# Kernel optimization log

Hardware: AMD Instinct MI355X
Metric: run time of the kernel (lower is better)

## Reference

```python
import jax, jax.numpy as jnp
import numpy as np

K = 10          # neighbors, hard-coded in MLP1.forward
NEG_SLOPE = 0.2 # LeakyReLU slope
EPS = 1e-5      # BatchNorm2d default eps


def setup_inputs() -> dict:
    key = jax.random.key(0)
    k1, k2, k3, k4 = jax.random.split(key, 4)
    B, C, N = 8, 6, 4096
    x = jax.random.normal(k1, (B, C, N), dtype=jnp.float32)
    W = jax.random.normal(k2, (64, 6), dtype=jnp.float32) * 0.2      # conv1x1 weight (O, I)
    gamma = jax.random.uniform(k3, (64,), jnp.float32, 0.5, 1.5)     # BN weight
    beta = jax.random.normal(k4, (64,), dtype=jnp.float32) * 0.1     # BN bias
    return {"x": x, "W": W, "gamma": gamma, "beta": beta}


def _knn_idx(x3, k):
    # pairwise_distance[b,i,j] = -||x_i - x_j||^2 (as in the torch knn)
    inner = jnp.einsum('bdn,bdm->bnm', x3, x3)          # x_i . x_j
    xx = jnp.sum(x3 * x3, axis=1)                       # (B, N)
    pd = 2.0 * inner - xx[:, :, None] - xx[:, None, :]  # (B, N, N)
    _, idx = jax.lax.top_k(pd, k)                       # k nearest (incl. self)
    return idx                                          # (B, N, k) int32


def reference(x, W, gamma, beta):
    # x: (B, 6, N)
    idx = _knn_idx(x[:, :3], K)                          # (B, N, k)
    # gather neighbor features: feat[b,c,n,j] = x[b,c,idx[b,n,j]]
    feat = jax.vmap(lambda xb, ib: xb[:, ib])(x, idx)    # (B, 6, N, k)
    # center xyz over the k neighbors and scale by 10
    xyz = feat[:, :3]
    xyz = (xyz - jnp.mean(xyz, axis=-1, keepdims=True)) * 10.0
    feat = jnp.concatenate([xyz, feat[:, 3:]], axis=1)   # (B, 6, N, k)
    # 1x1 conv (6 -> 64), no bias
    y = jnp.einsum('oc,bcnk->bonk', W, feat)             # (B, 64, N, k)
    # BatchNorm2d in train mode: batch stats over (B, N, k), biased variance
    mu = jnp.mean(y, axis=(0, 2, 3), keepdims=True)
    var = jnp.mean((y - mu) ** 2, axis=(0, 2, 3), keepdims=True)
    y = (y - mu) * jax.lax.rsqrt(var + EPS)
    y = y * gamma[None, :, None, None] + beta[None, :, None, None]
    # LeakyReLU(0.2)
    y = jnp.where(y >= 0, y, NEG_SLOPE * y)
    # max over neighbors k
    y = jnp.max(y, axis=-1)                              # (B, 64, N)
    # global max + mean pooling over N, concat along last axis
    x1 = jnp.max(y, axis=-1)                             # (B, 64)
    x2 = jnp.mean(y, axis=-1)                            # (B, 64)
    return jnp.concatenate([x1, x2], axis=-1)            # (B, 128)
```

## Files before the change

kernel.cpp:

```cpp
#include <hip/hip_runtime.h>
#include <float.h>

#define K_NN 10
#define BATCH 8
#define CIN 6
#define NPTS 4096
#define COUT 64
#define NSEG 8
#define SEGLEN (NPTS / NSEG)
#define CHUNK 16
#define NCHUNK (SEGLEN / CHUNK)
#define CAP 32
#define TPP 8
#define PPB2 32
#define SCAP 80
#define NEG_SLOPE 0.2f
#define BN_EPS 1e-5f

static constexpr size_t OFF_PTS2 = 0;
static constexpr size_t OFF_PTS  = OFF_PTS2 + (size_t)BATCH * NPTS * sizeof(float4);
static constexpr size_t OFF_Q    = OFF_PTS + (size_t)BATCH * NPTS * sizeof(float4);
static constexpr size_t SZ_Q     = (size_t)BATCH * NSEG * K_NN * NPTS * sizeof(int);
static constexpr size_t OFF_ST   = OFF_Q + SZ_Q;

__device__ __forceinline__ float wave_sum(float v) {
#pragma unroll
    for (int m = 32; m >= 1; m >>= 1) v += __shfl_xor(v, m, 64);
    return v;
}
__device__ __forceinline__ float wave_max(float v) {
#pragma unroll
    for (int m = 32; m >= 1; m >>= 1) v = fmaxf(v, __shfl_xor(v, m, 64));
    return v;
}

__device__ __forceinline__ float distp3(float qdx, float qdy, float qdz, float4 c) {
    return fmaf(qdx, c.x, fmaf(qdy, c.y, fmaf(qdz, c.z, -c.w)));
}

__device__ __forceinline__ void lex_insert(float (&vals)[K_NN], int (&inds)[K_NN],
                                           float d, int m) {
    if (d > vals[K_NN - 1] || (d == vals[K_NN - 1] && m < inds[K_NN - 1])) {
        vals[K_NN - 1] = d;
        inds[K_NN - 1] = m;
#pragma unroll
        for (int t = K_NN - 1; t > 0; t--) {
            if (vals[t] > vals[t - 1] ||
                (vals[t] == vals[t - 1] && inds[t] < inds[t - 1])) {
                float tv = vals[t]; vals[t] = vals[t - 1]; vals[t - 1] = tv;
                int ti = inds[t]; inds[t] = inds[t - 1]; inds[t - 1] = ti;
            }
        }
    }
}

__global__ __launch_bounds__(256) void prep_pts(const float* __restrict__ x,
                                                float4* __restrict__ pts,
                                                float4* __restrict__ pts2,
                                                double* __restrict__ stats) {
    if (blockIdx.x == 0 && threadIdx.x < 27) stats[threadIdx.x] = 0.0;
    int t = blockIdx.x * 256 + threadIdx.x;
    int b = t >> 12;
    int n = t & (NPTS - 1);
    const float* xb = x + (size_t)b * CIN * NPTS;
    float x0 = xb[n];
    float x1 = xb[NPTS + n];
    float x2 = xb[2 * NPTS + n];
    pts[t] = make_float4(x0, x1, x2, x0 * x0 + x1 * x1 + x2 * x2);
    pts2[t] = make_float4(xb[3 * NPTS + n], xb[4 * NPTS + n], xb[5 * NPTS + n], 0.f);
}

__global__ __launch_bounds__(256) void knn_part(const float4* __restrict__ pts,
                                                int* __restrict__ part) {
    __shared__ unsigned short ssm[CAP * 256];
    int b = blockIdx.y;
    int s = blockIdx.z;
    int n = blockIdx.x * 256 + threadIdx.x;
    const float4* p = pts + (size_t)b * NPTS;
    float4 qp = p[n];
    float qdx = 2.0f * qp.x, qdy = 2.0f * qp.y, qdz = 2.0f * qp.z;

    int m0 = s * SEGLEN;

    float vals[K_NN];
#pragma unroll
    for (int j = 0; j < K_NN; j++) vals[j] = -FLT_MAX;

    for (int ch = 0; ch < NCHUNK; ch++) {
        float cmax = -FLT_MAX;
#pragma unroll
        for (int u = 0; u < CHUNK; u++) {
            float4 c = p[m0 + ch * CHUNK + u];
            cmax = fmaxf(cmax, distp3(qdx, qdy, qdz, c));
        }
        float t = cmax;
#pragma unroll
        for (int j = 0; j < K_NN; j++) {
            float hi = fmaxf(vals[j], t);
            t = fminf(vals[j], t);
            vals[j] = hi;
        }
    }
    float thr = vals[K_NN - 1];

    int cnt = 0;
#pragma unroll 8
    for (int mm = 0; mm < SEGLEN; mm++) {
        float4 c = p[m0 + mm];
        float d = distp3(qdx, qdy, qdz, c);
        int slot = min(cnt, CAP - 1);
        ssm[slot * 256 + threadIdx.x] = (unsigned short)(m0 + mm);
        cnt += (d >= thr) ? 1 : 0;
    }

    float fv[K_NN];
    int fi[K_NN];
#pragma unroll
    for (int j = 0; j < K_NN; j++) { fv[j] = -FLT_MAX; fi[j] = 0; }

    if (cnt <= CAP) {
        for (int j = 0; j < cnt; j++) {
            int m = ssm[j * 256 + threadIdx.x];
            float4 c = p[m];
            float d = distp3(qdx, qdy, qdz, c);
            if (d > fv[K_NN - 1]) {
                fv[K_NN - 1] = d;
                fi[K_NN - 1] = m;
#pragma unroll
                for (int t2 = K_NN - 1; t2 > 0; t2--) {
                    if (fv[t2] > fv[t2 - 1]) {
                        float tv = fv[t2]; fv[t2] = fv[t2 - 1]; fv[t2 - 1] = tv;
                        int ti = fi[t2]; fi[t2] = fi[t2 - 1]; fi[t2 - 1] = ti;
                    }
                }
            }
        }
    } else {
        for (int mm = 0; mm < SEGLEN; mm++) {
            int m = m0 + mm;
            float4 c = p[m];
            float d = distp3(qdx, qdy, qdz, c);
            if (d > fv[K_NN - 1]) {
                fv[K_NN - 1] = d;
                fi[K_NN - 1] = m;
#pragma unroll
                for (int t2 = K_NN - 1; t2 > 0; t2--) {
                    if (fv[t2] > fv[t2 - 1]) {
                        float tv = fv[t2]; fv[t2] = fv[t2 - 1]; fv[t2 - 1] = tv;
                        int ti = fi[t2]; fi[t2] = fi[t2 - 1]; fi[t2 - 1] = ti;
                    }
                }
            }
        }
    }

    int* o = part + (((size_t)b * NSEG + s) * K_NN) * NPTS + n;
#pragma unroll
    for (int j = 0; j < K_NN; j++) o[(size_t)j * NPTS] = fi[j];
}

__global__ __launch_bounds__(256) void merge_feat(const float4* __restrict__ pts,
                                                  const float4* __restrict__ pts2,
                                                  const float* __restrict__ W,
                                                  const int* __restrict__ part,
                                                  float* __restrict__ q,
                                                  double* __restrict__ stats) {
    __shared__ float sW[COUT * CIN];
    __shared__ float sdv[PPB2][SCAP];
    __shared__ unsigned short smv[PPB2][SCAP];
    __shared__ int scnt[PPB2];
    __shared__ float sf[CIN][K_NN][PPB2];
    __shared__ float sred[4][27];

    int tid = threadIdx.x;
    int h = tid & (TPP - 1);
    int pt = tid >> 3;
    int b = blockIdx.y;
    int n = blockIdx.x * PPB2 + pt;

    for (int i = tid; i < COUT * CIN; i += 256) sW[i] = W[i];
    if (h == 0) scnt[pt] = 0;
    __syncthreads();

    const float4* p = pts + (size_t)b * NPTS;
    const float4* p2 = pts2 + (size_t)b * NPTS;
    float4 qp = p[n];
    float qdx = 2.0f * qp.x, qdy = 2.0f * qp.y, qdz = 2.0f * qp.z;

    const int* pp = part + (((size_t)b * NSEG + h) * K_NN) * NPTS + n;
    int ms[K_NN];
#pragma unroll
    for (int j = 0; j < K_NN; j++) ms[j] = pp[(size_t)j * NPTS];
    float ds[K_NN];
#pragma unroll
    for (int j = 0; j < K_NN; j++) ds[j] = distp3(qdx, qdy, qdz, p[ms[j]]);

    float t = ds[K_NN - 1];
    t = fmaxf(t, __shfl_xor(t, 1, 64));
    t = fmaxf(t, __shfl_xor(t, 2, 64));
    t = fmaxf(t, __shfl_xor(t, 4, 64));

#pragma unroll
    for (int j = 0; j < K_NN; j++) {
        if (ds[j] >= t) {
            int slot = atomicAdd(&scnt[pt], 1);
            sdv[pt][slot] = ds[j];
            smv[pt][slot] = (unsigned short)ms[j];
        } else break;
    }
    __syncthreads();

    int cnt = scnt[pt];
    float fv[K_NN];
    int fi[K_NN];
#pragma unroll
    for (int j = 0; j < K_NN; j++) { fv[j] = -FLT_MAX; fi[j] = 0x7FFFFFFF; }
    for (int i2 = 0; i2 < cnt; i2++)
        lex_insert(fv, fi, sdv[pt][i2], (int)smv[pt][i2]);

    for (int k = h; k < K_NN; k += TPP) {
        float4 c = p[fi[k]];
        float4 c2 = p2[fi[k]];
        sf[0][k][pt] = c.x; sf[1][k][pt] = c.y; sf[2][k][pt] = c.z;
        sf[3][k][pt] = c2.x; sf[4][k][pt] = c2.y; sf[5][k][pt] = c2.z;
    }
    __syncthreads();

    float mean[3];
#pragma unroll
    for (int c = 0; c < 3; c++) {
        float s = 0.f;
#pragma unroll
        for (int k = 0; k < K_NN; k++) s += sf[c][k][pt];
        mean[c] = s / 10.0f;
    }
    float f[CIN][K_NN];
#pragma unroll
    for (int c = 0; c < CIN; c++)
#pragma unroll
        for (int k = 0; k < K_NN; k++) {
            float v = sf[c][k][pt];
            f[c][k] = (c < 3) ? (v - mean[c]) * 10.0f : v;
        }

    float* qb = q + (size_t)b * 80 * NPTS + n;
#pragma unroll
    for (int oo = 0; oo < 8; oo++) {
        int o = h * 8 + oo;
        float w0 = sW[o * 6 + 0], w1 = sW[o * 6 + 1], w2 = sW[o * 6 + 2];
        float w3 = sW[o * 6 + 3], w4 = sW[o * 6 + 4], w5 = sW[o * 6 + 5];
        float mx = -FLT_MAX;
#pragma unroll
        for (int k = 0; k < K_NN; k++) {
            float y = w0 * f[0][k] + w1 * f[1][k] + w2 * f[2][k] +
                      w3 * f[3][k] + w4 * f[4][k] + w5 * f[5][k];
            mx = fmaxf(mx, y);
        }
        qb[(size_t)o * NPTS] = mx;
    }

    float s1[CIN];
    float s2[21];
#pragma unroll
    for (int c = 0; c < CIN; c++) s1[c] = 0.f;
#pragma unroll
    for (int i = 0; i < 21; i++) s2[i] = 0.f;
    if (h == 0) {
#pragma unroll
        for (int c = 0; c < CIN; c++) {
            float s = 0.f;
#pragma unroll
            for (int k = 0; k < K_NN; k++) s += f[c][k];
            s1[c] = s;
        }
#pragma unroll
        for (int k = 0; k < K_NN; k++) {
            int pp2 = 0;
#pragma unroll
            for (int c = 0; c < CIN; c++)
#pragma unroll
                for (int c2 = c; c2 < CIN; c2++) {
                    s2[pp2] += f[c][k] * f[c2][k];
                    pp2++;
                }
        }
    }
#pragma unroll
    for (int c = 0; c < CIN; c++) s1[c] = wave_sum(s1[c]);
#pragma unroll
    for (int i = 0; i < 21; i++) s2[i] = wave_sum(s2[i]);

    int wv = tid >> 6;
    int ln = tid & 63;
    if (ln == 0) {
#pragma unroll
        for (int c = 0; c < CIN; c++) sred[wv][c] = s1[c];
#pragma unroll
        for (int i = 0; i < 21; i++) sred[wv][6 + i] = s2[i];
    }
    __syncthreads();
    if (tid < 27) {
        float tt = sred[0][tid] + sred[1][tid] + sred[2][tid] + sred[3][tid];
        atomicAdd(&stats[tid], (double)tt);
    }
}

__global__ __launch_bounds__(256) void reduce_kernel(const float* __restrict__ q,
                                                     const double* __restrict__ stats,
                                                     const float* __restrict__ W,
                                                     const float* __restrict__ gamma,
                                                     const float* __restrict__ beta,
                                                     float* __restrict__ out) {
    int o = blockIdx.x;
    int b = blockIdx.y;

    const double minv = 1.0 / (double)((size_t)BATCH * NPTS * K_NN);
    double w[CIN];
#pragma unroll
    for (int c = 0; c < CIN; c++) w[c] = (double)W[o * CIN + c];
    double mu = 0.0;
#pragma unroll
    for (int c = 0; c < CIN; c++) mu += w[c] * stats[c];
    mu *= minv;
    double ey2 = 0.0;
    int pidx = 6;
#pragma unroll
    for (int c = 0; c < CIN; c++)
#pragma unroll
        for (int c2 = c; c2 < CIN; c2++) {
            double v = w[c] * w[c2] * stats[pidx];
            ey2 += (c2 == c) ? v : 2.0 * v;
            pidx++;
        }
    ey2 *= minv;
    double var = ey2 - mu * mu;
    float scale = gamma[o] * rsqrtf((float)var + BN_EPS);
    float shift = beta[o] - (float)mu * scale;

    const float* qp = q + ((size_t)b * 80 + o) * NPTS;
    float mx = -FLT_MAX, sm = 0.f;
    for (int i = threadIdx.x; i < NPTS; i += 256) {
        float z = scale * qp[i] + shift;
        z = (z >= 0.f) ? z : NEG_SLOPE * z;
        mx = fmaxf(mx, z);
        sm += z;
    }
    mx = wave_max(mx);
    sm = wave_sum(sm);
    __shared__ float smx[4], ssm2[4];
    int wv = threadIdx.x >> 6;
    int ln = threadIdx.x & 63;
    if (ln == 0) { smx[wv] = mx; ssm2[wv] = sm; }
    __syncthreads();
    if (threadIdx.x == 0) {
        float m = fmaxf(fmaxf(smx[0], smx[1]), fmaxf(smx[2], smx[3]));
        float s = ssm2[0] + ssm2[1] + ssm2[2] + ssm2[3];
        out[b * 2 * COUT + o] = m;
        out[b * 2 * COUT + COUT + o] = s * (1.0f / (float)NPTS);
    }
}

extern "C" void kernel_launch(void* const* d_in, const int* in_sizes, int n_in,
                              void* d_out, int out_size, void* d_ws, size_t ws_size,
                              hipStream_t stream) {
    const float* x     = (const float*)d_in[0];
    const float* W     = (const float*)d_in[1];
    const float* gamma = (const float*)d_in[2];
    const float* beta  = (const float*)d_in[3];
    float* out = (float*)d_out;

    char* ws = (char*)d_ws;
    float4* pts2  = (float4*)(ws + OFF_PTS2);
    float4* pts   = (float4*)(ws + OFF_PTS);
    int*    part  = (int*)(ws + OFF_Q);
    float*  q     = (float*)(ws + OFF_Q);
    double* stats = (double*)(ws + OFF_ST);

    prep_pts<<<BATCH * NPTS / 256, 256, 0, stream>>>(x, pts, pts2, stats);
    knn_part<<<dim3(NPTS / 256, BATCH, NSEG), 256, 0, stream>>>(pts, part);
    merge_feat<<<dim3(NPTS / PPB2, BATCH), 256, 0, stream>>>(pts, pts2, W, part, q, stats);
    reduce_kernel<<<dim3(COUT, BATCH), 256, 0, stream>>>(q, stats, W, gamma, beta, out);
}
```

Baseline: 203.3 us.

## Fuse four kernels into one cooperative persistent kernel with grid syncs

Merges the prep, kNN partial, merge/feature and reduce kernels into one cooperative kernel whose stages are separated by grid-wide syncs, with the shared memory of each stage overlaid in a union. The goal is to remove the launch gaps and tail drain between the four kernels. If there are not enough co-resident blocks, it launches with 512 blocks or falls back to separate launches. The fused kernel adds the cost of grid.sync barriers and host-side occupancy queries on every call, and the launch bound of 4 blocks per CU may limit registers in the kNN stage.

```diff
diff --git a/kernel.cpp b/kernel.cpp
--- a/kernel.cpp
+++ b/kernel.cpp
@@ -1,5 +1,8 @@
 #include <hip/hip_runtime.h>
+#include <hip/hip_cooperative_groups.h>
 #include <float.h>
+
+namespace cg = cooperative_groups;
 
 #define K_NN 10
 #define BATCH 8
@@ -54,12 +57,25 @@
     }
 }
 
-__global__ __launch_bounds__(256) void prep_pts(const float* __restrict__ x,
-                                                float4* __restrict__ pts,
-                                                float4* __restrict__ pts2,
-                                                double* __restrict__ stats) {
-    if (blockIdx.x == 0 && threadIdx.x < 27) stats[threadIdx.x] = 0.0;
-    int t = blockIdx.x * 256 + threadIdx.x;
+union SharedU {
+    struct { unsigned short ssm[CAP * 256]; } a;
+    struct {
+        float sW[COUT * CIN];
+        float sdv[PPB2][SCAP];
+        unsigned short smv[PPB2][SCAP];
+        int scnt[PPB2];
+        float sf[CIN][K_NN][PPB2];
+        float sred[4][27];
+    } b;
+    struct { float smx[4]; float ssm2[4]; } c;
+};
+
+__device__ __forceinline__ void phaseP(int g, int tid, const float* __restrict__ x,
+                                       float4* __restrict__ pts,
+                                       float4* __restrict__ pts2,
+                                       double* __restrict__ stats) {
+    if (g == 0 && tid < 27) stats[tid] = 0.0;
+    int t = g * 256 + tid;
     int b = t >> 12;
     int n = t & (NPTS - 1);
     const float* xb = x + (size_t)b * CIN * NPTS;
@@ -70,12 +86,13 @@
     pts2[t] = make_float4(xb[3 * NPTS + n], xb[4 * NPTS + n], xb[5 * NPTS + n], 0.f);
 }
 
-__global__ __launch_bounds__(256) void knn_part(const float4* __restrict__ pts,
-                                                int* __restrict__ part) {
-    __shared__ unsigned short ssm[CAP * 256];
-    int b = blockIdx.y;
-    int s = blockIdx.z;
-    int n = blockIdx.x * 256 + threadIdx.x;
+__device__ __forceinline__ void phaseA(int g, int tid,
+                                       const float4* __restrict__ pts,
+                                       int* __restrict__ part, SharedU& sh) {
+    int nblk = g & 15;
+    int b = (g >> 4) & 7;
+    int s = g >> 7;
+    int n = nblk * 256 + tid;
     const float4* p = pts + (size_t)b * NPTS;
     float4 qp = p[n];
     float qdx = 2.0f * qp.x, qdy = 2.0f * qp.y, qdz = 2.0f * qp.z;
@@ -109,7 +126,7 @@
         float4 c = p[m0 + mm];
         float d = distp3(qdx, qdy, qdz, c);
         int slot = min(cnt, CAP - 1);
-        ssm[slot * 256 + threadIdx.x] = (unsigned short)(m0 + mm);
+        sh.a.ssm[slot * 256 + tid] = (unsigned short)(m0 + mm);
         cnt += (d >= thr) ? 1 : 0;
     }
 
@@ -120,7 +137,7 @@
 
     if (cnt <= CAP) {
         for (int j = 0; j < cnt; j++) {
-            int m = ssm[j * 256 + threadIdx.x];
+            int m = sh.a.ssm[j * 256 + tid];
             float4 c = p[m];
             float d = distp3(qdx, qdy, qdz, c);
             if (d > fv[K_NN - 1]) {
@@ -159,27 +176,21 @@
     for (int j = 0; j < K_NN; j++) o[(size_t)j * NPTS] = fi[j];
 }
 
-__global__ __launch_bounds__(256) void merge_feat(const float4* __restrict__ pts,
-                                                  const float4* __restrict__ pts2,
-                                                  const float* __restrict__ W,
-                                                  const int* __restrict__ part,
-                                                  float* __restrict__ q,
-                                                  double* __restrict__ stats) {
-    __shared__ float sW[COUT * CIN];
-    __shared__ float sdv[PPB2][SCAP];
-    __shared__ unsigned short smv[PPB2][SCAP];
-    __shared__ int scnt[PPB2];
-    __shared__ float sf[CIN][K_NN][PPB2];
-    __shared__ float sred[4][27];
-
-    int tid = threadIdx.x;
+__device__ __forceinline__ void phaseB(int g, int tid,
+                                       const float4* __restrict__ pts,
+                                       const float4* __restrict__ pts2,
+                                       const float* __restrict__ W,
+                                       const int* __restrict__ part,
+                                       float* __restrict__ q,
+                                       double* __restrict__ stats, SharedU& sh) {
     int h = tid & (TPP - 1);
     int pt = tid >> 3;
-    int b = blockIdx.y;
-    int n = blockIdx.x * PPB2 + pt;
-
-    for (int i = tid; i < COUT * CIN; i += 256) sW[i] = W[i];
-    if (h == 0) scnt[pt] = 0;
+    int nblk2 = g & 127;
+    int b = g >> 7;
+    int n = nblk2 * PPB2 + pt;
+
+    for (int i = tid; i < COUT * CIN; i += 256) sh.b.sW[i] = W[i];
+    if (h == 0) sh.b.scnt[pt] = 0;
     __syncthreads();
 
     const float4* p = pts + (size_t)b * NPTS;
@@ -203,26 +214,26 @@
 #pragma unroll
     for (int j = 0; j < K_NN; j++) {
         if (ds[j] >= t) {
-            int slot = atomicAdd(&scnt[pt], 1);
-            sdv[pt][slot] = ds[j];
-            smv[pt][slot] = (unsigned short)ms[j];
+            int slot = atomicAdd(&sh.b.scnt[pt], 1);
+            sh.b.sdv[pt][slot] = ds[j];
+            sh.b.smv[pt][slot] = (unsigned short)ms[j];
         } else break;
     }
     __syncthreads();
 
-    int cnt = scnt[pt];
+    int cnt = sh.b.scnt[pt];
     float fv[K_NN];
     int fi[K_NN];
 #pragma unroll
     for (int j = 0; j < K_NN; j++) { fv[j] = -FLT_MAX; fi[j] = 0x7FFFFFFF; }
     for (int i2 = 0; i2 < cnt; i2++)
-        lex_insert(fv, fi, sdv[pt][i2], (int)smv[pt][i2]);
+        lex_insert(fv, fi, sh.b.sdv[pt][i2], (int)sh.b.smv[pt][i2]);
 
     for (int k = h; k < K_NN; k += TPP) {
         float4 c = p[fi[k]];
         float4 c2 = p2[fi[k]];
-        sf[0][k][pt] = c.x; sf[1][k][pt] = c.y; sf[2][k][pt] = c.z;
-        sf[3][k][pt] = c2.x; sf[4][k][pt] = c2.y; sf[5][k][pt] = c2.z;
+        sh.b.sf[0][k][pt] = c.x; sh.b.sf[1][k][pt] = c.y; sh.b.sf[2][k][pt] = c.z;
+        sh.b.sf[3][k][pt] = c2.x; sh.b.sf[4][k][pt] = c2.y; sh.b.sf[5][k][pt] = c2.z;
     }
     __syncthreads();
 
@@ -231,7 +242,7 @@
     for (int c = 0; c < 3; c++) {
         float s = 0.f;
 #pragma unroll
-        for (int k = 0; k < K_NN; k++) s += sf[c][k][pt];
+        for (int k = 0; k < K_NN; k++) s += sh.b.sf[c][k][pt];
         mean[c] = s / 10.0f;
     }
     float f[CIN][K_NN];
@@ -239,7 +250,7 @@
     for (int c = 0; c < CIN; c++)
 #pragma unroll
         for (int k = 0; k < K_NN; k++) {
-            float v = sf[c][k][pt];
+            float v = sh.b.sf[c][k][pt];
             f[c][k] = (c < 3) ? (v - mean[c]) * 10.0f : v;
         }
 
@@ -247,8 +258,8 @@
 #pragma unroll
     for (int oo = 0; oo < 8; oo++) {
         int o = h * 8 + oo;
-        float w0 = sW[o * 6 + 0], w1 = sW[o * 6 + 1], w2 = sW[o * 6 + 2];
-        float w3 = sW[o * 6 + 3], w4 = sW[o * 6 + 4], w5 = sW[o * 6 + 5];
+        float w0 = sh.b.sW[o * 6 + 0], w1 = sh.b.sW[o * 6 + 1], w2 = sh.b.sW[o * 6 + 2];
+        float w3 = sh.b.sW[o * 6 + 3], w4 = sh.b.sW[o * 6 + 4], w5 = sh.b.sW[o * 6 + 5];
         float mx = -FLT_MAX;
 #pragma unroll
         for (int k = 0; k < K_NN; k++) {
@@ -294,25 +305,28 @@
     int ln = tid & 63;
     if (ln == 0) {
 #pragma unroll
-        for (int c = 0; c < CIN; c++) sred[wv][c] = s1[c];
-#pragma unroll
-        for (int i = 0; i < 21; i++) sred[wv][6 + i] = s2[i];
+        for (int c = 0; c < CIN; c++) sh.b.sred[wv][c] = s1[c];
+#pragma unroll
+        for (int i = 0; i < 21; i++) sh.b.sred[wv][6 + i] = s2[i];
     }
     __syncthreads();
     if (tid < 27) {
-        float tt = sred[0][tid] + sred[1][tid] + sred[2][tid] + sred[3][tid];
+        float tt = sh.b.sred[0][tid] + sh.b.sred[1][tid] +
+                   sh.b.sred[2][tid] + sh.b.sred[3][tid];
         atomicAdd(&stats[tid], (double)tt);
     }
-}
-
-__global__ __launch_bounds__(256) void reduce_kernel(const float* __restrict__ q,
-                                                     const double* __restrict__ stats,
-                                                     const float* __restrict__ W,
-                                                     const float* __restrict__ gamma,
-                                                     const float* __restrict__ beta,
-                                                     float* __restrict__ out) {
-    int o = blockIdx.x;
-    int b = blockIdx.y;
+    __syncthreads();
+}
+
+__device__ __forceinline__ void phaseC(int g, int tid,
+                                       const float* __restrict__ q,
+                                       const double* __restrict__ stats,
+                                       const float* __restrict__ W,
+                                       const float* __restrict__ gamma,
+                                       const float* __restrict__ beta,
+                                       float* __restrict__ out, SharedU& sh) {
+    int o = g & 63;
+    int b = g >> 6;
 
     const double minv = 1.0 / (double)((size_t)BATCH * NPTS * K_NN);
     double w[CIN];
@@ -339,7 +353,7 @@
 
     const float* qp = q + ((size_t)b * 80 + o) * NPTS;
     float mx = -FLT_MAX, sm = 0.f;
-    for (int i = threadIdx.x; i < NPTS; i += 256) {
+    for (int i = tid; i < NPTS; i += 256) {
         float z = scale * qp[i] + shift;
         z = (z >= 0.f) ? z : NEG_SLOPE * z;
         mx = fmaxf(mx, z);
@@ -347,17 +361,74 @@
     }
     mx = wave_max(mx);
     sm = wave_sum(sm);
-    __shared__ float smx[4], ssm2[4];
-    int wv = threadIdx.x >> 6;
-    int ln = threadIdx.x & 63;
-    if (ln == 0) { smx[wv] = mx; ssm2[wv] = sm; }
-    __syncthreads();
-    if (threadIdx.x == 0) {
-        float m = fmaxf(fmaxf(smx[0], smx[1]), fmaxf(smx[2], smx[3]));
-        float s = ssm2[0] + ssm2[1] + ssm2[2] + ssm2[3];
+    int wv = tid >> 6;
+    int ln = tid & 63;
+    if (ln == 0) { sh.c.smx[wv] = mx; sh.c.ssm2[wv] = sm; }
+    __syncthreads();
+    if (tid == 0) {
+        float m = fmaxf(fmaxf(sh.c.smx[0], sh.c.smx[1]),
+                        fmaxf(sh.c.smx[2], sh.c.smx[3]));
+        float s = sh.c.ssm2[0] + sh.c.ssm2[1] + sh.c.ssm2[2] + sh.c.ssm2[3];
         out[b * 2 * COUT + o] = m;
         out[b * 2 * COUT + COUT + o] = s * (1.0f / (float)NPTS);
     }
+    __syncthreads();
+}
+
+__global__ __launch_bounds__(256, 4) void fused_kernel(
+        const float* __restrict__ x, const float* __restrict__ W,
+        const float* __restrict__ gamma, const float* __restrict__ beta,
+        float* __restrict__ out,
+        float4* __restrict__ pts, float4* __restrict__ pts2,
+        int* __restrict__ part, float* __restrict__ q,
+        double* __restrict__ stats) {
+    __shared__ SharedU sh;
+    cg::grid_group grid = cg::this_grid();
+    int tid = threadIdx.x;
+    int gd = gridDim.x;
+
+    for (int t = blockIdx.x; t < 128; t += gd) phaseP(t, tid, x, pts, pts2, stats);
+    __threadfence();
+    grid.sync();
+    for (int t = blockIdx.x; t < 1024; t += gd) phaseA(t, tid, pts, part, sh);
+    __threadfence();
+    grid.sync();
+    for (int t = blockIdx.x; t < 1024; t += gd)
+        phaseB(t, tid, pts, pts2, W, part, q, stats, sh);
+    __threadfence();
+    grid.sync();
+    for (int t = blockIdx.x; t < 512; t += gd)
+        phaseC(t, tid, q, stats, W, gamma, beta, out, sh);
+}
+
+__global__ __launch_bounds__(256) void kP(const float* __restrict__ x,
+                                          float4* __restrict__ pts,
+                                          float4* __restrict__ pts2,
+                                          double* __restrict__ stats) {
+    phaseP(blockIdx.x, threadIdx.x, x, pts, pts2, stats);
+}
+__global__ __launch_bounds__(256) void kA(const float4* __restrict__ pts,
+                                          int* __restrict__ part) {
+    __shared__ SharedU sh;
+    phaseA(blockIdx.x, threadIdx.x, pts, part, sh);
+}
+__global__ __launch_bounds__(256) void kB(const float4* __restrict__ pts,
+                                          const float4* __restrict__ pts2,
+                                          const float* __restrict__ W,
+                                          const int* __restrict__ part,
+                                          float* __restrict__ q,
+                                          double* __restrict__ stats) {
+    __shared__ SharedU sh;
+    phaseB(blockIdx.x, threadIdx.x, pts, pts2, W, part, q, stats, sh);
+}
+__global__ __launch_bounds__(256) void kC(const float* __restrict__ q,
+                                          const double* __restrict__ stats,
+                                          const float* __restrict__ W,
+                                          const float* __restrict__ gamma,
+                                          const float* __restrict__ beta,
+                                          float* __restrict__ out) {
+    __shared__ SharedU sh;
+    phaseC(blockIdx.x, threadIdx.x, q, stats, W, gamma, beta, out, sh);
 }
 
 extern "C" void kernel_launch(void* const* d_in, const int* in_sizes, int n_in,
@@ -376,8 +447,32 @@
     float*  q     = (float*)(ws + OFF_Q);
     double* stats = (double*)(ws + OFF_ST);
 
-    prep_pts<<<BATCH * NPTS / 256, 256, 0, stream>>>(x, pts, pts2, stats);
-    knn_part<<<dim3(NPTS / 256, BATCH, NSEG), 256, 0, stream>>>(pts, part);
-    merge_feat<<<dim3(NPTS / PPB2, BATCH), 256, 0, stream>>>(pts, pts2, W, part, q, stats);
-    reduce_kernel<<<dim3(COUT, BATCH), 256, 0, stream>>>(q, stats, W, gamma, beta, out);
-}
+    int blocksPerCU = 0;
+    hipError_t qe = hipOccupancyMaxActiveBlocksPerMultiprocessor(
+        &blocksPerCU, (const void*)fused_kernel, 256, 0);
+    int numCU = 0;
+    if (hipDeviceGetAttribute(&numCU, hipDeviceAttributeMultiprocessorCount, 0)
+        != hipSuccess || numCU <= 0) numCU = 256;
+    long coopCap = (qe == hipSuccess) ? (long)blocksPerCU * numCU : 0;
+
+    void* args[] = {(void*)&x, (void*)&W, (void*)&gamma, (void*)&beta, (void*)&out,
+                    (void*)&pts, (void*)&pts2, (void*)&part, (void*)&q, (void*)&stats};
+
+    bool done = false;
+    if (coopCap >= 1024) {
+        done = (hipLaunchCooperativeKernel((const void*)fused_kernel, dim3(1024),
+                                           dim3(256), args, 0, stream) == hipSuccess);
+        if (!done) (void)hipGetLastError();
+    }
+    if (!done && coopCap >= 512) {
+        done = (hipLaunchCooperativeKernel((const void*)fused_kernel, dim3(512),
+                                           dim3(256), args, 0, stream) == hipSuccess);
+        if (!done) (void)hipGetLastError();
+    }
+    if (!done) {
+        kP<<<128, 256, 0, stream>>>(x, pts, pts2, stats);
+        kA<<<1024, 256, 0, stream>>>(pts, part);
+        kB<<<1024, 256, 0, stream>>>(pts, pts2, W, part, q, stats);
+        kC<<<512, 256, 0, stream>>>(q, stats, W, gamma, beta, out);
+    }
+}
```

Result: slower. 568.4 us (+179.6%).
